# Kernel tuning notes

Hardware: AMD Instinct MI355X
Metric: run time of the kernel (lower is better)

Reference implementation:

```python
import jax, jax.numpy as jnp
import numpy as np

NUM_EMBEDDINGS = 1024
EMBEDDING_DIM = 256
COMMITMENT_COST = 0.25


def setup_inputs() -> dict:
    key = jax.random.key(0)
    k1, k2 = jax.random.split(key)
    z_e = jax.random.normal(k1, (32, EMBEDDING_DIM, 32, 32), dtype=jnp.float32)
    # nn.Embedding weight init: uniform(-1/K, 1/K)
    embedding = jax.random.uniform(
        k2, (NUM_EMBEDDINGS, EMBEDDING_DIM), dtype=jnp.float32,
        minval=-1.0 / NUM_EMBEDDINGS, maxval=1.0 / NUM_EMBEDDINGS)
    return {"z_e": z_e, "embedding": embedding}


def reference(z_e, embedding):
    B, D, H, W = z_e.shape
    K = embedding.shape[0]
    sg = jax.lax.stop_gradient

    z = jnp.transpose(z_e, (0, 2, 3, 1))            # (B, H, W, D)
    flat = z.reshape(-1, D)                          # (N, D), N = B*H*W

    distances = (jnp.sum(flat * flat, axis=1, keepdims=True)
                 + jnp.sum(embedding * embedding, axis=1)
                 - 2.0 * flat @ embedding.T)

    encoding_indices = jnp.argmin(distances, axis=1)  # (N,)
    # one_hot @ embedding == direct gather of nearest code vectors
    z_q_flat = embedding[encoding_indices]            # (N, D)
    z_q = z_q_flat.reshape(z.shape)                   # (B, H, W, D)

    e_latent_loss = jnp.mean((sg(z_q) - z) ** 2)
    q_latent_loss = jnp.mean((z_q - sg(z)) ** 2)
    loss = q_latent_loss + COMMITMENT_COST * e_latent_loss

    # straight-through estimator
    z_q_st = z + sg(z_q - z)
    z_q_out = jnp.transpose(z_q_st, (0, 3, 1, 2))     # (B, D, H, W)

    # avg_probs = mean over N of one-hot == histogram of indices / N
    N = flat.shape[0]
    counts = jnp.zeros((K,), dtype=jnp.float32).at[encoding_indices].add(1.0)
    avg_probs = counts / N
    perplexity = jnp.exp(-jnp.sum(avg_probs * jnp.log(avg_probs + 1e-10)))

    return (z_q_out, loss, perplexity, encoding_indices, distances)
```

## Files before the change

kernel.cpp:

```cpp
#include <hip/hip_runtime.h>
#include <cfloat>

typedef __attribute__((ext_vector_type(8))) short bf16x8;
typedef __attribute__((ext_vector_type(4))) float f32x4;
typedef __attribute__((ext_vector_type(8))) unsigned short u16x8;

#define NROW 32768
#define ZQ_OFF   0
#define LOSS_OFF 8388608
#define PERP_OFF 8388609
#define IDX_OFF  8388610
#define DIST_OFF 8421378

#define WSB_AHI  0x0
#define WSB_BHI  0x1000000
#define WSB_RN   0x2100000
#define WSB_EN   0x2120000
#define WSB_PKEY 0x2200000
#define WSB_CNT  0x2620000
#define WSB_LOSS 0x2621000

__device__ __forceinline__ float sq_rn(float x) { return __fmul_rn(x, x); }

__device__ __forceinline__ unsigned enc_f(float f) {
  unsigned u = __float_as_uint(f);
  return (u & 0x80000000u) ? ~u : (u | 0x80000000u);
}
__device__ __forceinline__ float dec_f(unsigned e) {
  unsigned u = (e & 0x80000000u) ? (e ^ 0x80000000u) : ~e;
  return __uint_as_float(u);
}

__device__ __forceinline__ unsigned short bf16_rne(float f) {
  unsigned u = __float_as_uint(f);
  unsigned r = u + 0x7fffu + ((u >> 16) & 1u);
  return (unsigned short)(r >> 16);
}

__device__ __forceinline__ void gload16(const void* g, void* l) {
  __builtin_amdgcn_global_load_lds(
      (const __attribute__((address_space(1))) unsigned int*)g,
      (__attribute__((address_space(3))) unsigned int*)l, 16, 0, 0);
}

__device__ float pairwise_norm256(const float* __restrict__ p, int stride) {
  float h[2];
#pragma unroll
  for (int half = 0; half < 2; ++half) {
    const float* q = p + (size_t)half * 128 * stride;
    float r[8];
#pragma unroll
    for (int j = 0; j < 8; ++j) r[j] = sq_rn(q[(size_t)j * stride]);
    for (int d8 = 8; d8 < 128; d8 += 8) {
#pragma unroll
      for (int j = 0; j < 8; ++j)
        r[j] = __fadd_rn(r[j], sq_rn(q[(size_t)(d8 + j) * stride]));
    }
    h[half] = __fadd_rn(__fadd_rn(__fadd_rn(r[0], r[1]), __fadd_rn(r[2], r[3])),
                        __fadd_rn(__fadd_rn(r[4], r[5]), __fadd_rn(r[6], r[7])));
  }
  return __fadd_rn(h[0], h[1]);
}

__launch_bounds__(256)
__global__ void prepE_kernel(const float* __restrict__ emb,
                             unsigned short* __restrict__ bhi,
                             float* __restrict__ embnorm) {
  if (blockIdx.x >= 128) {
    const int k = ((blockIdx.x - 128) << 8) + threadIdx.x;
    embnorm[k] = pairwise_norm256(emb + ((size_t)k << 8), 1);
    return;
  }
  const int tg = (blockIdx.x << 8) + threadIdx.x;
  const int k = tg >> 5, cd = tg & 31;
  const float4 v0 = *(const float4*)(emb + ((size_t)k << 8) + cd * 8);
  const float4 v1 = *(const float4*)(emb + ((size_t)k << 8) + cd * 8 + 4);
  const float xs[8] = {v0.x, v0.y, v0.z, v0.w, v1.x, v1.y, v1.z, v1.w};
  u16x8 vh;
#pragma unroll
  for (int u = 0; u < 8; ++u) vh[u] = (short)bf16_rne(xs[u]);
  const size_t pos = (((size_t)(k >> 7)) << 12) + ((size_t)(cd >> 3) << 10)
                   + ((size_t)(k & 127) << 3) + (size_t)((cd & 7) ^ (k & 7));
  *(u16x8*)(bhi + pos * 8) = vh;
}

__launch_bounds__(256)
__global__ void prep_kernel(const float* __restrict__ z_e,
                            unsigned short* __restrict__ ahi,
                            float* __restrict__ rownorm) {
  __shared__ float xt[64][132];
  __shared__ float hs[128][2];
  const int t = threadIdx.x;
  const int ntile = blockIdx.x;
  const int n0 = ntile << 7;
  const int b = n0 >> 10, s0 = n0 & 1023;
  const size_t zb = ((size_t)b << 18) + (size_t)s0;
  const int myhalf = t >> 7;
  const int mys = t & 127;
  float r[8];
#pragma unroll
  for (int j = 0; j < 8; ++j) r[j] = 0.f;
  for (int dt = 0; dt < 4; ++dt) {
#pragma unroll
    for (int p = 0; p < 8; ++p) {
      const int idx = (p << 8) + t;
      const int dd = idx >> 5;
      const int sq = (idx & 31) << 2;
      const float4 v = *(const float4*)(z_e + zb + ((size_t)((dt << 6) + dd) << 10) + sq);
      const int sw = ((dd >> 3) & 3) << 3;
      *(float4*)(&xt[dd][sq ^ sw]) = v;
    }
    __syncthreads();
    if ((dt >> 1) == myhalf) {
#pragma unroll
      for (int g = 0; g < 8; ++g) {
        const int col = mys ^ ((g & 3) << 3);
#pragma unroll
        for (int j = 0; j < 8; ++j)
          r[j] = __fadd_rn(r[j], sq_rn(xt[(g << 3) + j][col]));
      }
    }
#pragma unroll
    for (int p = 0; p < 4; ++p) {
      const int idx = (p << 8) + t;
      const int s = idx >> 3, c = idx & 7;
      const int sw = (c & 3) << 3;
      u16x8 vh;
#pragma unroll
      for (int u = 0; u < 8; ++u)
        vh[u] = (short)bf16_rne(xt[(c << 3) + u][s ^ sw]);
      const size_t pos = ((size_t)ntile << 12) + ((size_t)dt << 10)
                       + (size_t)(s << 3) + (size_t)(c ^ (s & 7));
      *(u16x8*)(ahi + pos * 8) = vh;
    }
    __syncthreads();
  }
  const float h = __fadd_rn(__fadd_rn(__fadd_rn(r[0], r[1]), __fadd_rn(r[2], r[3])),
                            __fadd_rn(__fadd_rn(r[4], r[5]), __fadd_rn(r[6], r[7])));
  hs[mys][myhalf] = h;
  __syncthreads();
  if (t < 128) rownorm[n0 + t] = __fadd_rn(hs[t][0], hs[t][1]);
}

#define LDS_A 0
#define LDS_B 16384

__launch_bounds__(256, 4)
__global__ void dist_kernel(const unsigned short* __restrict__ ahi,
                            const unsigned short* __restrict__ bhi,
                            const float* __restrict__ rownorm,
                            const float* __restrict__ embnorm,
                            float* __restrict__ dist,
                            unsigned long long* __restrict__ pkey) {
  __shared__ char lds[32768];
  const int tid = threadIdx.x;
  const int lane = tid & 63;
  const int wv = tid >> 6;
  const int wr = wv >> 1, wc = wv & 1;
  const int bid = blockIdx.x;
  const int xcd = bid & 7;
  const int jj = bid >> 3;
  const int ntile = (xcd << 5) + (jj >> 3);
  const int ktile = jj & 7;

  const unsigned short* gsrc = (wv < 2) ? ahi + ((size_t)ntile << 15)
                                        : bhi + ((size_t)ktile << 15);
  char* ldsBase = lds + ((wv >> 1) << 14);

  f32x4 acc[4][4];
#pragma unroll
  for (int i = 0; i < 4; ++i)
#pragma unroll
    for (int j = 0; j < 4; ++j) acc[i][j] = (f32x4){0.f, 0.f, 0.f, 0.f};

  for (int s = 0; s < 4; ++s) {
    {
      const unsigned short* g = gsrc + ((size_t)s << 13);
#pragma unroll
      for (int q = 0; q < 8; ++q) {
        const int cq = ((wv & 1) << 3) + q;
        gload16(g + ((size_t)(cq * 64 + lane) << 3), ldsBase + cq * 1024);
      }
    }
    __syncthreads();
#pragma unroll
    for (int half = 0; half < 2; ++half) {
      const int kb = half << 2;
      bf16x8 ah[4], bh[4];
#pragma unroll
      for (int i = 0; i < 4; ++i) {
        const int row = (wr << 6) + (i << 4) + (lane & 15);
        const int ch = (kb + (lane >> 4)) ^ (row & 7);
        ah[i] = *(const bf16x8*)(lds + LDS_A + ((row << 3) + ch) * 16);
      }
#pragma unroll
      for (int j = 0; j < 4; ++j) {
        const int row = (wc << 6) + (j << 4) + (lane & 15);
        const int ch = (kb + (lane >> 4)) ^ (row & 7);
        bh[j] = *(const bf16x8*)(lds + LDS_B + ((row << 3) + ch) * 16);
      }
#pragma unroll
      for (int i = 0; i < 4; ++i)
#pragma unroll
        for (int j = 0; j < 4; ++j)
          acc[i][j] = __builtin_amdgcn_mfma_f32_16x16x32_bf16(ah[i], bh[j], acc[i][j], 0, 0, 0);
    }
    __syncthreads();
  }
  const int n0 = (ntile << 7) + (wr << 6);
  const int k0 = (ktile << 7) + (wc << 6);
  const int g = lane >> 4, tl = lane & 15;
  const int tileidx = (ktile << 1) + wc;
  float en[4];
#pragma unroll
  for (int j = 0; j < 4; ++j) en[j] = embnorm[k0 + (j << 4) + tl];
#pragma unroll
  for (int i = 0; i < 4; ++i) {
#pragma unroll
    for (int r = 0; r < 4; ++r) {
      const int n = n0 + (i << 4) + (g << 2) + r;
      const float rn = rownorm[n];
      float* drow = dist + (size_t)n * 1024 + k0 + tl;
      unsigned long long key = ~0ULL;
#pragma unroll
      for (int j = 0; j < 4; ++j) {
        const float dv = __fsub_rn(__fadd_rn(rn, en[j]), __fmul_rn(2.0f, acc[i][j][r]));
        drow[j << 4] = dv;
        const unsigned long long c =
            ((unsigned long long)enc_f(dv) << 32) | (unsigned)(k0 + (j << 4) + tl);
        key = c < key ? c : key;
      }
#pragma unroll
      for (int mm = 1; mm < 16; mm <<= 1) {
        const unsigned long long o = __shfl_xor(key, mm, 64);
        key = o < key ? o : key;
      }
      if (tl == 0) pkey[(size_t)n * 16 + tileidx] = key;
    }
  }
}

__launch_bounds__(256)
__global__ void rzq_kernel(const float* __restrict__ z_e,
                           const float* __restrict__ emb,
                           const float* __restrict__ rownorm,
                           const float* __restrict__ embnorm,
                           const float* __restrict__ dist,
                           const unsigned long long* __restrict__ pkey,
                           float* __restrict__ out,
                           float* __restrict__ counts,
                           float* __restrict__ lossacc) {
  __shared__ float xl[16][260];
  __shared__ int bk_s[16];
  __shared__ float wredf[4];
  const int t = threadIdx.x;
  const int s0 = blockIdx.x << 4;
  const int b = s0 >> 10, sb = s0 & 1023;
  {
    const int d = t >> 2;
    const int s4 = (t & 3) << 2;
#pragma unroll
    for (int p = 0; p < 4; ++p) {
      const int dd = d + p * 64;
      const float4 v = *(const float4*)(z_e + ((size_t)b << 18) + ((size_t)dd << 10) + sb + s4);
      xl[s4 + 0][dd] = v.x; xl[s4 + 1][dd] = v.y;
      xl[s4 + 2][dd] = v.z; xl[s4 + 3][dd] = v.w;
    }
  }
  __syncthreads();
  const int wv = t >> 6, lane = t & 63;
  for (int rr = 0; rr < 4; ++rr) {
    const int srow = (wv << 2) + rr;
    const int n = s0 + srow;
    const unsigned long long mypk = (lane < 16) ? pkey[(size_t)n * 16 + lane] : ~0ULL;
    unsigned long long key = mypk;
#pragma unroll
    for (int mm = 1; mm < 64; mm <<= 1) {
      const unsigned long long o = __shfl_xor(key, mm, 64);
      key = o < key ? o : key;
    }
    const float v1 = dec_f((unsigned)(key >> 32));
    const unsigned ue = (__float_as_uint(v1) >> 23) & 0xffu;
    const float ulp = __uint_as_float((ue - 23) << 23);
    const float w = v1 + 2.0f * ulp + 3e-3f;
    unsigned qmask = (unsigned)(__ballot(dec_f((unsigned)(mypk >> 32)) <= w) & 0xffffULL);
    const float rn = rownorm[n];
    const float4 xv = *(const float4*)(&xl[srow][lane << 2]);
    unsigned long long best = ~0ULL;
    while (qmask) {
      const int T = __ffs(qmask) - 1;
      qmask &= qmask - 1;
      const float dval = dist[(size_t)n * 1024 + T * 64 + lane];
      unsigned long long cm = __ballot(dval <= w);
      while (cm) {
        const int l2 = __ffsll(cm) - 1;
        cm &= cm - 1;
        const int kk = T * 64 + l2;
        const float4 ev = *(const float4*)(emb + ((size_t)kk << 8) + (lane << 2));
        double p = (double)xv.x * ev.x + (double)xv.y * ev.y
                 + (double)xv.z * ev.z + (double)xv.w * ev.w;
#pragma unroll
        for (int mm = 1; mm < 64; mm <<= 1) p += __shfl_xor(p, mm, 64);
        const float dotf = (float)p;
        const float D = __fsub_rn(__fadd_rn(rn, embnorm[kk]), __fmul_rn(2.0f, dotf));
        const unsigned long long c = ((unsigned long long)enc_f(D) << 32) | (unsigned)kk;
        best = c < best ? c : best;
      }
    }
    const int bestk = (int)(best & 0xffffffffu);
    if (lane == 0) {
      bk_s[srow] = bestk;
      out[IDX_OFF + n] = (float)bestk;
      atomicAdd(&counts[bestk], 1.0f);
    }
  }
  __syncthreads();
  const int d = t;
  float zq[16];
  float lsum = 0.f;
#pragma unroll
  for (int r2 = 0; r2 < 16; ++r2) {
    const float e = emb[((size_t)bk_s[r2] << 8) + d];
    const float z = xl[r2][d];
    const float df = __fsub_rn(e, z);
    zq[r2] = __fadd_rn(z, df);
    lsum = fmaf(df, df, lsum);
  }
  float* op = out + ZQ_OFF + ((size_t)b << 18) + ((size_t)d << 10) + sb;
#pragma unroll
  for (int q = 0; q < 4; ++q)
    *(float4*)(op + (q << 2)) =
        make_float4(zq[q * 4], zq[q * 4 + 1], zq[q * 4 + 2], zq[q * 4 + 3]);
#pragma unroll
  for (int m = 32; m > 0; m >>= 1) lsum += __shfl_xor(lsum, m, 64);
  if (lane == 0) wredf[wv] = lsum;
  __syncthreads();
  if (t == 0) atomicAdd(lossacc, wredf[0] + wredf[1] + wredf[2] + wredf[3]);
}

__launch_bounds__(256)
__global__ void final_kernel(const float* __restrict__ counts, const float* __restrict__ lossacc,
                             float* __restrict__ out) {
  const int t = threadIdx.x;
  float ssum = 0.f;
#pragma unroll
  for (int u = 0; u < 4; ++u) {
    const float p = counts[t * 4 + u] * (1.0f / 32768.0f);
    ssum += p * logf(p + 1e-10f);
  }
#pragma unroll
  for (int m = 32; m > 0; m >>= 1) ssum += __shfl_xor(ssum, m, 64);
  __shared__ float wred[4];
  if ((t & 63) == 0) wred[t >> 6] = ssum;
  __syncthreads();
  if (t == 0) {
    const float tot = wred[0] + wred[1] + wred[2] + wred[3];
    out[PERP_OFF] = expf(-tot);
    const float mql = lossacc[0] * (1.0f / 8388608.0f);
    out[LOSS_OFF] = __fadd_rn(mql, __fmul_rn(0.25f, mql));
  }
}

extern "C" void kernel_launch(void* const* d_in, const int* in_sizes, int n_in,
                              void* d_out, int out_size, void* d_ws, size_t ws_size,
                              hipStream_t stream) {
  const float* z_e = (const float*)d_in[0];
  const float* emb = (const float*)d_in[1];
  float* out = (float*)d_out;
  char* ws = (char*)d_ws;

  unsigned short* ahi = (unsigned short*)(ws + WSB_AHI);
  unsigned short* bhi = (unsigned short*)(ws + WSB_BHI);
  float* rownorm = (float*)(ws + WSB_RN);
  float* embnorm = (float*)(ws + WSB_EN);
  unsigned long long* pkey = (unsigned long long*)(ws + WSB_PKEY);
  float* counts = (float*)(ws + WSB_CNT);
  float* lossacc = (float*)(ws + WSB_LOSS);

  hipMemsetAsync(ws + WSB_CNT, 0, 4100, stream);

  hipLaunchKernelGGL(prepE_kernel, dim3(132), dim3(256), 0, stream, emb, bhi, embnorm);
  hipLaunchKernelGGL(prep_kernel, dim3(256), dim3(256), 0, stream, z_e, ahi, rownorm);
  hipLaunchKernelGGL(dist_kernel, dim3(2048), dim3(256), 0, stream,
                     ahi, bhi, rownorm, embnorm, out + DIST_OFF, pkey);
  hipLaunchKernelGGL(rzq_kernel, dim3(2048), dim3(256), 0, stream,
                     z_e, emb, rownorm, embnorm, out + DIST_OFF, pkey, out, counts, lossacc);
  hipLaunchKernelGGL(final_kernel, dim3(1), dim3(256), 0, stream, counts, lossacc, out);
}
```

Before: 132.5 us.

## Fuse z_e prep into distance GEMM and fold final reduction into rzq

The separate prep kernel that wrote bf16 A tiles to global memory is merged into the distance kernel. Each 512-thread block now transposes and converts its 128-row z_e tile into LDS, keeps the A fragments in registers, and sweeps all 1024 codes with double-buffered B tiles. The memset and the final perplexity kernel are removed: prepE zeroes the counters, and the last rzq block, detected with an atomic ticket, computes loss and perplexity. This cuts launches and the A round trip through global memory, but it drops to 256 large blocks, which lowers parallelism and occupancy.

```diff
diff --git a/kernel.cpp b/kernel.cpp
--- a/kernel.cpp
+++ b/kernel.cpp
@@ -12,13 +12,13 @@
 #define IDX_OFF  8388610
 #define DIST_OFF 8421378
 
-#define WSB_AHI  0x0
-#define WSB_BHI  0x1000000
-#define WSB_RN   0x2100000
-#define WSB_EN   0x2120000
-#define WSB_PKEY 0x2200000
-#define WSB_CNT  0x2620000
-#define WSB_LOSS 0x2621000
+#define WSB_BHI  0x0
+#define WSB_RN   0x100000
+#define WSB_EN   0x120000
+#define WSB_PKEY 0x200000
+#define WSB_CNT  0xA00000
+#define WSB_LOSS 0xA01000
+#define WSB_CTR  0xA01004
 
 __device__ __forceinline__ float sq_rn(float x) { return __fmul_rn(x, x); }
 
@@ -65,7 +65,12 @@
 __launch_bounds__(256)
 __global__ void prepE_kernel(const float* __restrict__ emb,
                              unsigned short* __restrict__ bhi,
-                             float* __restrict__ embnorm) {
+                             float* __restrict__ embnorm,
+                             float* __restrict__ zero_region) {
+  if (blockIdx.x == 132) {
+    for (int i = threadIdx.x; i < 1026; i += 256) zero_region[i] = 0.f;
+    return;
+  }
   if (blockIdx.x >= 128) {
     const int k = ((blockIdx.x - 128) << 8) + threadIdx.x;
     embnorm[k] = pairwise_norm256(emb + ((size_t)k << 8), 1);
@@ -84,17 +89,33 @@
   *(u16x8*)(bhi + pos * 8) = vh;
 }
 
-__launch_bounds__(256)
-__global__ void prep_kernel(const float* __restrict__ z_e,
-                            unsigned short* __restrict__ ahi,
-                            float* __restrict__ rownorm) {
-  __shared__ float xt[64][132];
-  __shared__ float hs[128][2];
+#define LA   0
+#define LXT  65536
+#define LB0  65536
+#define LB1  81920
+#define LHS  99328
+#define LRNL 100352
+#define LDS_TOT 100864
+
+__launch_bounds__(512, 2)
+__global__ void dist_kernel(const float* __restrict__ z_e,
+                            const unsigned short* __restrict__ bhi,
+                            const float* __restrict__ embnorm,
+                            float* __restrict__ rownorm,
+                            float* __restrict__ dist,
+                            unsigned long long* __restrict__ pkey) {
+  __shared__ char lds[LDS_TOT];
+  float* xt = (float*)(lds + LXT);
+  float* hs = (float*)(lds + LHS);
+  float* rnl = (float*)(lds + LRNL);
   const int t = threadIdx.x;
+  const int lane = t & 63, wv = t >> 6;
+  const int g = lane >> 4, tl = lane & 15;
   const int ntile = blockIdx.x;
   const int n0 = ntile << 7;
-  const int b = n0 >> 10, s0 = n0 & 1023;
-  const size_t zb = ((size_t)b << 18) + (size_t)s0;
+  const int bb = n0 >> 10, s0 = n0 & 1023;
+  const size_t zb = ((size_t)bb << 18) + (size_t)s0;
+
   const int myhalf = t >> 7;
   const int mys = t & 127;
   float r[8];
@@ -102,140 +123,143 @@
   for (int j = 0; j < 8; ++j) r[j] = 0.f;
   for (int dt = 0; dt < 4; ++dt) {
 #pragma unroll
-    for (int p = 0; p < 8; ++p) {
-      const int idx = (p << 8) + t;
+    for (int p = 0; p < 4; ++p) {
+      const int idx = (p << 9) + t;
       const int dd = idx >> 5;
       const int sq = (idx & 31) << 2;
       const float4 v = *(const float4*)(z_e + zb + ((size_t)((dt << 6) + dd) << 10) + sq);
       const int sw = ((dd >> 3) & 3) << 3;
-      *(float4*)(&xt[dd][sq ^ sw]) = v;
+      *(float4*)(&xt[dd * 132 + (sq ^ sw)]) = v;
     }
     __syncthreads();
-    if ((dt >> 1) == myhalf) {
-#pragma unroll
-      for (int g = 0; g < 8; ++g) {
-        const int col = mys ^ ((g & 3) << 3);
+    if (t < 256 && (dt >> 1) == myhalf) {
+#pragma unroll
+      for (int gg = 0; gg < 8; ++gg) {
+        const int col = mys ^ ((gg & 3) << 3);
 #pragma unroll
         for (int j = 0; j < 8; ++j)
-          r[j] = __fadd_rn(r[j], sq_rn(xt[(g << 3) + j][col]));
+          r[j] = __fadd_rn(r[j], sq_rn(xt[((gg << 3) + j) * 132 + col]));
       }
     }
 #pragma unroll
-    for (int p = 0; p < 4; ++p) {
-      const int idx = (p << 8) + t;
-      const int s = idx >> 3, c = idx & 7;
-      const int sw = (c & 3) << 3;
+    for (int p = 0; p < 2; ++p) {
+      const int idx = (p << 9) + t;
+      const int s = idx >> 3, cc = idx & 7;
+      const int sw = (cc & 3) << 3;
       u16x8 vh;
 #pragma unroll
       for (int u = 0; u < 8; ++u)
-        vh[u] = (short)bf16_rne(xt[(c << 3) + u][s ^ sw]);
-      const size_t pos = ((size_t)ntile << 12) + ((size_t)dt << 10)
-                       + (size_t)(s << 3) + (size_t)(c ^ (s & 7));
-      *(u16x8*)(ahi + pos * 8) = vh;
+        vh[u] = (short)bf16_rne(xt[((cc << 3) + u) * 132 + (s ^ sw)]);
+      const int c = (dt << 3) + cc;
+      const int cs = (c & 0x18) | ((c & 7) ^ (s & 7));
+      *(u16x8*)(lds + LA + (s << 9) + (cs << 4)) = vh;
     }
     __syncthreads();
   }
-  const float h = __fadd_rn(__fadd_rn(__fadd_rn(r[0], r[1]), __fadd_rn(r[2], r[3])),
-                            __fadd_rn(__fadd_rn(r[4], r[5]), __fadd_rn(r[6], r[7])));
-  hs[mys][myhalf] = h;
-  __syncthreads();
-  if (t < 128) rownorm[n0 + t] = __fadd_rn(hs[t][0], hs[t][1]);
-}
-
-#define LDS_A 0
-#define LDS_B 16384
-
-__launch_bounds__(256, 4)
-__global__ void dist_kernel(const unsigned short* __restrict__ ahi,
-                            const unsigned short* __restrict__ bhi,
-                            const float* __restrict__ rownorm,
-                            const float* __restrict__ embnorm,
-                            float* __restrict__ dist,
-                            unsigned long long* __restrict__ pkey) {
-  __shared__ char lds[32768];
-  const int tid = threadIdx.x;
-  const int lane = tid & 63;
-  const int wv = tid >> 6;
-  const int wr = wv >> 1, wc = wv & 1;
-  const int bid = blockIdx.x;
-  const int xcd = bid & 7;
-  const int jj = bid >> 3;
-  const int ntile = (xcd << 5) + (jj >> 3);
-  const int ktile = jj & 7;
-
-  const unsigned short* gsrc = (wv < 2) ? ahi + ((size_t)ntile << 15)
-                                        : bhi + ((size_t)ktile << 15);
-  char* ldsBase = lds + ((wv >> 1) << 14);
-
-  f32x4 acc[4][4];
+  if (t < 256) {
+    const float h = __fadd_rn(__fadd_rn(__fadd_rn(r[0], r[1]), __fadd_rn(r[2], r[3])),
+                              __fadd_rn(__fadd_rn(r[4], r[5]), __fadd_rn(r[6], r[7])));
+    hs[(mys << 1) + myhalf] = h;
+  }
+  __syncthreads();
+  if (t < 128) {
+    const float rn = __fadd_rn(hs[t << 1], hs[(t << 1) + 1]);
+    rnl[t] = rn;
+    rownorm[n0 + t] = rn;
+  }
+
+  const int wr = wv >> 2, wc = wv & 3;
+  bf16x8 areg[4][8];
+#pragma unroll
+  for (int cidx = 0; cidx < 8; ++cidx) {
+#pragma unroll
+    for (int i = 0; i < 4; ++i) {
+      const int row = (wr << 6) + (i << 4) + tl;
+      const int c0 = (cidx << 2) + g;
+      const int cs = (c0 & 0x18) | ((c0 & 7) ^ (row & 7));
+      areg[i][cidx] = *(const bf16x8*)(lds + LA + (row << 9) + (cs << 4));
+    }
+  }
+  f32x4 acc[4][2];
 #pragma unroll
   for (int i = 0; i < 4; ++i)
 #pragma unroll
-    for (int j = 0; j < 4; ++j) acc[i][j] = (f32x4){0.f, 0.f, 0.f, 0.f};
-
-  for (int s = 0; s < 4; ++s) {
-    {
-      const unsigned short* g = gsrc + ((size_t)s << 13);
-#pragma unroll
-      for (int q = 0; q < 8; ++q) {
-        const int cq = ((wv & 1) << 3) + q;
-        gload16(g + ((size_t)(cq * 64 + lane) << 3), ldsBase + cq * 1024);
+    for (int j = 0; j < 2; ++j) acc[i][j] = (f32x4){0.f, 0.f, 0.f, 0.f};
+  char* const bufs[2] = {lds + LB0, lds + LB1};
+  {
+#pragma unroll
+    for (int q = 0; q < 2; ++q) {
+      const int ch = (wv << 7) + (q << 6) + lane;
+      gload16(bhi + ((size_t)ch << 3), bufs[0] + (ch << 4));
+    }
+  }
+  __syncthreads();
+  for (int kt = 0; kt < 8; ++kt) {
+#pragma unroll
+    for (int s = 0; s < 4; ++s) {
+      const int m = (kt << 2) + s;
+      if (m < 31) {
+        const unsigned short* src = bhi + ((size_t)(m + 1) << 13);
+        char* dstb = bufs[(s + 1) & 1];
+#pragma unroll
+        for (int q = 0; q < 2; ++q) {
+          const int ch = (wv << 7) + (q << 6) + lane;
+          gload16(src + ((size_t)ch << 3), dstb + (ch << 4));
+        }
       }
-    }
-    __syncthreads();
-#pragma unroll
-    for (int half = 0; half < 2; ++half) {
-      const int kb = half << 2;
-      bf16x8 ah[4], bh[4];
-#pragma unroll
-      for (int i = 0; i < 4; ++i) {
-        const int row = (wr << 6) + (i << 4) + (lane & 15);
-        const int ch = (kb + (lane >> 4)) ^ (row & 7);
-        ah[i] = *(const bf16x8*)(lds + LDS_A + ((row << 3) + ch) * 16);
+      const char* bbuf = bufs[s & 1];
+#pragma unroll
+      for (int half = 0; half < 2; ++half) {
+        bf16x8 bh[2];
+#pragma unroll
+        for (int j = 0; j < 2; ++j) {
+          const int row = (wc << 5) + (j << 4) + tl;
+          const int chs = ((half << 2) + g) ^ (row & 7);
+          bh[j] = *(const bf16x8*)(bbuf + (row << 7) + (chs << 4));
+        }
+#pragma unroll
+        for (int i = 0; i < 4; ++i)
+#pragma unroll
+          for (int j = 0; j < 2; ++j)
+            acc[i][j] = __builtin_amdgcn_mfma_f32_16x16x32_bf16(
+                areg[i][(s << 1) + half], bh[j], acc[i][j], 0, 0, 0);
       }
-#pragma unroll
-      for (int j = 0; j < 4; ++j) {
-        const int row = (wc << 6) + (j << 4) + (lane & 15);
-        const int ch = (kb + (lane >> 4)) ^ (row & 7);
-        bh[j] = *(const bf16x8*)(lds + LDS_B + ((row << 3) + ch) * 16);
+      if (s == 3) {
+        const int k0 = (kt << 7) + (wc << 5);
+        float en[2];
+#pragma unroll
+        for (int j = 0; j < 2; ++j) en[j] = embnorm[k0 + (j << 4) + tl];
+#pragma unroll
+        for (int i = 0; i < 4; ++i) {
+#pragma unroll
+          for (int rr = 0; rr < 4; ++rr) {
+            const int lrow = (wr << 6) + (i << 4) + (g << 2) + rr;
+            const int n = n0 + lrow;
+            const float rn = rnl[lrow];
+            float* drow = dist + (size_t)n * 1024 + k0 + tl;
+            unsigned long long key = ~0ULL;
+#pragma unroll
+            for (int j = 0; j < 2; ++j) {
+              const float dv = __fsub_rn(__fadd_rn(rn, en[j]), __fmul_rn(2.0f, acc[i][j][rr]));
+              drow[j << 4] = dv;
+              const unsigned long long c =
+                  ((unsigned long long)enc_f(dv) << 32) | (unsigned)(k0 + (j << 4) + tl);
+              key = c < key ? c : key;
+            }
+#pragma unroll
+            for (int mm = 1; mm < 16; mm <<= 1) {
+              const unsigned long long o = __shfl_xor(key, mm, 64);
+              key = o < key ? o : key;
+            }
+            if (tl == 0) pkey[((size_t)n << 5) + (kt << 2) + wc] = key;
+          }
+        }
+#pragma unroll
+        for (int i = 0; i < 4; ++i)
+#pragma unroll
+          for (int j = 0; j < 2; ++j) acc[i][j] = (f32x4){0.f, 0.f, 0.f, 0.f};
       }
-#pragma unroll
-      for (int i = 0; i < 4; ++i)
-#pragma unroll
-        for (int j = 0; j < 4; ++j)
-          acc[i][j] = __builtin_amdgcn_mfma_f32_16x16x32_bf16(ah[i], bh[j], acc[i][j], 0, 0, 0);
-    }
-    __syncthreads();
-  }
-  const int n0 = (ntile << 7) + (wr << 6);
-  const int k0 = (ktile << 7) + (wc << 6);
-  const int g = lane >> 4, tl = lane & 15;
-  const int tileidx = (ktile << 1) + wc;
-  float en[4];
-#pragma unroll
-  for (int j = 0; j < 4; ++j) en[j] = embnorm[k0 + (j << 4) + tl];
-#pragma unroll
-  for (int i = 0; i < 4; ++i) {
-#pragma unroll
-    for (int r = 0; r < 4; ++r) {
-      const int n = n0 + (i << 4) + (g << 2) + r;
-      const float rn = rownorm[n];
-      float* drow = dist + (size_t)n * 1024 + k0 + tl;
-      unsigned long long key = ~0ULL;
-#pragma unroll
-      for (int j = 0; j < 4; ++j) {
-        const float dv = __fsub_rn(__fadd_rn(rn, en[j]), __fmul_rn(2.0f, acc[i][j][r]));
-        drow[j << 4] = dv;
-        const unsigned long long c =
-            ((unsigned long long)enc_f(dv) << 32) | (unsigned)(k0 + (j << 4) + tl);
-        key = c < key ? c : key;
-      }
-#pragma unroll
-      for (int mm = 1; mm < 16; mm <<= 1) {
-        const unsigned long long o = __shfl_xor(key, mm, 64);
-        key = o < key ? o : key;
-      }
-      if (tl == 0) pkey[(size_t)n * 16 + tileidx] = key;
+      __syncthreads();
     }
   }
 }
@@ -249,10 +273,12 @@
                            const unsigned long long* __restrict__ pkey,
                            float* __restrict__ out,
                            float* __restrict__ counts,
-                           float* __restrict__ lossacc) {
+                           float* __restrict__ lossacc,
+                           unsigned* __restrict__ ctr) {
   __shared__ float xl[16][260];
   __shared__ int bk_s[16];
   __shared__ float wredf[4];
+  __shared__ unsigned lastblk;
   const int t = threadIdx.x;
   const int s0 = blockIdx.x << 4;
   const int b = s0 >> 10, sb = s0 & 1023;
@@ -272,7 +298,7 @@
   for (int rr = 0; rr < 4; ++rr) {
     const int srow = (wv << 2) + rr;
     const int n = s0 + srow;
-    const unsigned long long mypk = (lane < 16) ? pkey[(size_t)n * 16 + lane] : ~0ULL;
+    const unsigned long long mypk = (lane < 32) ? pkey[((size_t)n << 5) + lane] : ~0ULL;
     unsigned long long key = mypk;
 #pragma unroll
     for (int mm = 1; mm < 64; mm <<= 1) {
@@ -283,19 +309,19 @@
     const unsigned ue = (__float_as_uint(v1) >> 23) & 0xffu;
     const float ulp = __uint_as_float((ue - 23) << 23);
     const float w = v1 + 2.0f * ulp + 3e-3f;
-    unsigned qmask = (unsigned)(__ballot(dec_f((unsigned)(mypk >> 32)) <= w) & 0xffffULL);
+    unsigned qmask = (unsigned)(__ballot(dec_f((unsigned)(mypk >> 32)) <= w) & 0xffffffffULL);
     const float rn = rownorm[n];
     const float4 xv = *(const float4*)(&xl[srow][lane << 2]);
     unsigned long long best = ~0ULL;
     while (qmask) {
       const int T = __ffs(qmask) - 1;
       qmask &= qmask - 1;
-      const float dval = dist[(size_t)n * 1024 + T * 64 + lane];
-      unsigned long long cm = __ballot(dval <= w);
+      const float dval = dist[(size_t)n * 1024 + T * 32 + (lane & 31)];
+      unsigned long long cm = __ballot(dval <= w) & 0xffffffffULL;
       while (cm) {
         const int l2 = __ffsll(cm) - 1;
         cm &= cm - 1;
-        const int kk = T * 64 + l2;
+        const int kk = T * 32 + l2;
         const float4 ev = *(const float4*)(emb + ((size_t)kk << 8) + (lane << 2));
         double p = (double)xv.x * ev.x + (double)xv.y * ev.y
                  + (double)xv.z * ev.z + (double)xv.w * ev.w;
@@ -315,48 +341,51 @@
     }
   }
   __syncthreads();
-  const int d = t;
-  float zq[16];
-  float lsum = 0.f;
-#pragma unroll
-  for (int r2 = 0; r2 < 16; ++r2) {
-    const float e = emb[((size_t)bk_s[r2] << 8) + d];
-    const float z = xl[r2][d];
-    const float df = __fsub_rn(e, z);
-    zq[r2] = __fadd_rn(z, df);
-    lsum = fmaf(df, df, lsum);
-  }
-  float* op = out + ZQ_OFF + ((size_t)b << 18) + ((size_t)d << 10) + sb;
-#pragma unroll
-  for (int q = 0; q < 4; ++q)
-    *(float4*)(op + (q << 2)) =
-        make_float4(zq[q * 4], zq[q * 4 + 1], zq[q * 4 + 2], zq[q * 4 + 3]);
-#pragma unroll
-  for (int m = 32; m > 0; m >>= 1) lsum += __shfl_xor(lsum, m, 64);
-  if (lane == 0) wredf[wv] = lsum;
-  __syncthreads();
-  if (t == 0) atomicAdd(lossacc, wredf[0] + wredf[1] + wredf[2] + wredf[3]);
-}
-
-__launch_bounds__(256)
-__global__ void final_kernel(const float* __restrict__ counts, const float* __restrict__ lossacc,
-                             float* __restrict__ out) {
-  const int t = threadIdx.x;
+  {
+    const int d = t;
+    float zq[16];
+    float lsum = 0.f;
+#pragma unroll
+    for (int r2 = 0; r2 < 16; ++r2) {
+      const float e = emb[((size_t)bk_s[r2] << 8) + d];
+      const float z = xl[r2][d];
+      const float df = __fsub_rn(e, z);
+      zq[r2] = __fadd_rn(z, df);
+      lsum = fmaf(df, df, lsum);
+    }
+    float* op = out + ZQ_OFF + ((size_t)b << 18) + ((size_t)d << 10) + sb;
+#pragma unroll
+    for (int q = 0; q < 4; ++q)
+      *(float4*)(op + (q << 2)) =
+          make_float4(zq[q * 4], zq[q * 4 + 1], zq[q * 4 + 2], zq[q * 4 + 3]);
+#pragma unroll
+    for (int m = 32; m > 0; m >>= 1) lsum += __shfl_xor(lsum, m, 64);
+    if (lane == 0) wredf[wv] = lsum;
+  }
+  __syncthreads();
+  if (t == 0) {
+    atomicAdd(lossacc, wredf[0] + wredf[1] + wredf[2] + wredf[3]);
+    __threadfence();
+    lastblk = (atomicAdd(ctr, 1u) == 2047u) ? 1u : 0u;
+  }
+  __syncthreads();
+  if (!lastblk) return;
   float ssum = 0.f;
 #pragma unroll
   for (int u = 0; u < 4; ++u) {
-    const float p = counts[t * 4 + u] * (1.0f / 32768.0f);
+    const float cv = atomicAdd(&counts[(u << 8) + t], 0.0f);
+    const float p = cv * (1.0f / 32768.0f);
     ssum += p * logf(p + 1e-10f);
   }
 #pragma unroll
   for (int m = 32; m > 0; m >>= 1) ssum += __shfl_xor(ssum, m, 64);
-  __shared__ float wred[4];
-  if ((t & 63) == 0) wred[t >> 6] = ssum;
+  __shared__ float wred2[4];
+  if ((t & 63) == 0) wred2[t >> 6] = ssum;
   __syncthreads();
   if (t == 0) {
-    const float tot = wred[0] + wred[1] + wred[2] + wred[3];
+    const float tot = wred2[0] + wred2[1] + wred2[2] + wred2[3];
     out[PERP_OFF] = expf(-tot);
-    const float mql = lossacc[0] * (1.0f / 8388608.0f);
+    const float mql = atomicAdd(lossacc, 0.0f) * (1.0f / 8388608.0f);
     out[LOSS_OFF] = __fadd_rn(mql, __fmul_rn(0.25f, mql));
   }
 }
@@ -369,21 +398,19 @@
   float* out = (float*)d_out;
   char* ws = (char*)d_ws;
 
-  unsigned short* ahi = (unsigned short*)(ws + WSB_AHI);
   unsigned short* bhi = (unsigned short*)(ws + WSB_BHI);
   float* rownorm = (float*)(ws + WSB_RN);
   float* embnorm = (float*)(ws + WSB_EN);
   unsigned long long* pkey = (unsigned long long*)(ws + WSB_PKEY);
   float* counts = (float*)(ws + WSB_CNT);
   float* lossacc = (float*)(ws + WSB_LOSS);
-
-  hipMemsetAsync(ws + WSB_CNT, 0, 4100, stream);
-
-  hipLaunchKernelGGL(prepE_kernel, dim3(132), dim3(256), 0, stream, emb, bhi, embnorm);
-  hipLaunchKernelGGL(prep_kernel, dim3(256), dim3(256), 0, stream, z_e, ahi, rownorm);
-  hipLaunchKernelGGL(dist_kernel, dim3(2048), dim3(256), 0, stream,
-                     ahi, bhi, rownorm, embnorm, out + DIST_OFF, pkey);
+  unsigned* ctr = (unsigned*)(ws + WSB_CTR);
+
+  hipLaunchKernelGGL(prepE_kernel, dim3(133), dim3(256), 0, stream,
+                     emb, bhi, embnorm, counts);
+  hipLaunchKernelGGL(dist_kernel, dim3(256), dim3(512), 0, stream,
+                     z_e, bhi, embnorm, rownorm, out + DIST_OFF, pkey);
   hipLaunchKernelGGL(rzq_kernel, dim3(2048), dim3(256), 0, stream,
-                     z_e, emb, rownorm, embnorm, out + DIST_OFF, pkey, out, counts, lossacc);
-  hipLaunchKernelGGL(final_kernel, dim3(1), dim3(256), 0, stream, counts, lossacc, out);
-}
+                     z_e, emb, rownorm, embnorm, out + DIST_OFF, pkey,
+                     out, counts, lossacc, ctr);
+}
```

Result: slower. 204.2 us (+54.1%).
